# Performance work log

Hardware: AMD Instinct MI355X
Metric: run time of the kernel (lower is better)

The kernel has to match this reference:

```python
import jax, jax.numpy as jnp
import numpy as np

N_ATOM_FEATS = 64
N_RBF = 10
N_CONV = 3
N_HIDDEN = 64
N_NODES = 50000
N_EDGES = 800000
N_GRAPHS = 512


def setup_inputs() -> dict:
    key = jax.random.key(0)
    ks = jax.random.split(key, 32)
    d = {}
    d["x_ids"] = jax.random.randint(ks[0], (N_NODES,), 0, 95)
    d["edge_index"] = jax.random.randint(ks[1], (2, N_EDGES), 0, N_NODES)
    d["edge_attr"] = jax.random.uniform(ks[2], (N_EDGES,), jnp.float32) * 6.0  # distances in [0,6)
    d["batch"] = jnp.sort(jax.random.randint(ks[3], (N_NODES,), 0, N_GRAPHS))
    # parameters
    def lin(k, fan_in, shape):
        return jax.random.normal(k, shape, jnp.float32) / np.sqrt(fan_in)
    d["emb"] = jax.random.normal(ks[4], (95, N_ATOM_FEATS), jnp.float32)
    d["blk_W1"] = lin(ks[5], N_ATOM_FEATS, (N_CONV, N_ATOM_FEATS, N_ATOM_FEATS))
    d["blk_b1"] = jnp.zeros((N_CONV, N_ATOM_FEATS), jnp.float32)
    d["blk_We"] = lin(ks[6], N_RBF, (N_CONV, N_RBF, N_ATOM_FEATS))
    d["blk_be"] = jnp.zeros((N_CONV, N_ATOM_FEATS), jnp.float32)
    d["blk_W2"] = lin(ks[7], N_ATOM_FEATS, (N_CONV, N_ATOM_FEATS, N_ATOM_FEATS))
    d["blk_b2"] = jnp.zeros((N_CONV, N_ATOM_FEATS), jnp.float32)
    d["Ws"] = lin(ks[8], N_ATOM_FEATS, (N_ATOM_FEATS, 2 * N_HIDDEN))
    d["bs"] = jnp.zeros((2 * N_HIDDEN,), jnp.float32)
    d["Wbg1"] = lin(ks[9], 2 * N_HIDDEN, (2 * N_HIDDEN, N_HIDDEN))
    d["bbg1"] = jnp.zeros((N_HIDDEN,), jnp.float32)
    d["Wbg2"] = lin(ks[10], N_HIDDEN, (N_HIDDEN, 1))
    d["bbg2"] = jnp.zeros((1,), jnp.float32)
    d["Weh1"] = lin(ks[11], 2 * N_HIDDEN, (2 * N_HIDDEN, N_HIDDEN))
    d["beh1"] = jnp.zeros((N_HIDDEN,), jnp.float32)
    d["Weh2"] = lin(ks[12], N_HIDDEN, (N_HIDDEN, 1))
    d["beh2"] = jnp.zeros((1,), jnp.float32)
    return d


def reference(x_ids, edge_index, edge_attr, batch, emb,
              blk_W1, blk_b1, blk_We, blk_be, blk_W2, blk_b2,
              Ws, bs, Wbg1, bbg1, Wbg2, bbg2, Weh1, beh1, Weh2, beh2):
    src, dst = edge_index[0], edge_index[1]
    # embedding lookup [N, F]
    x = emb[x_ids]
    # Gaussian smearing RBF: [E, n_rbf]
    offset = jnp.linspace(0.0, 6.0, N_RBF).astype(edge_attr.dtype)
    coeff = -0.5 / (offset[1] - offset[0]) ** 2
    e = jnp.exp(coeff * (edge_attr[:, None] - offset) ** 2)
    # interaction blocks (SchNet-style CFConv with residual)
    for i in range(N_CONV):
        h = x @ blk_W1[i] + blk_b1[i]                     # [N, F]
        f = e @ blk_We[i] + blk_be[i]                     # [E, F] edge filters
        m = h[src] * f                                    # [E, F] messages
        agg = jax.ops.segment_sum(m, dst, num_segments=N_NODES)
        x = x + agg @ blk_W2[i] + blk_b2[i]
        x = jax.nn.softplus(x)
    # global mean pool over graphs
    sums = jax.ops.segment_sum(x, batch, num_segments=N_GRAPHS)
    cnts = jax.ops.segment_sum(jnp.ones((x.shape[0],), x.dtype), batch, num_segments=N_GRAPHS)
    c = sums / jnp.maximum(cnts, 1.0)[:, None]
    c = jax.nn.relu(c @ Ws + bs)                          # [G, 2H]
    out_bg = jax.nn.relu(c @ Wbg1 + bbg1) @ Wbg2 + bbg2   # [G, 1]
    out_eh = jax.nn.relu(c @ Weh1 + beh1) @ Weh2 + beh2   # [G, 1]
    return (out_bg, out_eh)
```

## Files before the change

kernel.cpp:

```cpp
#include <hip/hip_runtime.h>
#include <hip/hip_fp16.h>
#include <cstddef>


#define BSH 8

#define RBF_C0 1.0f
#define RBF_C1 0.60653065971f
#define RBF_C2 0.13533528324f
#define RBF_C3 0.011108996538f
#define RBF_C4 3.3546262790e-4f
#define RBF_C5 3.7266531720e-6f
#define RBF_C6 1.5229979745e-8f
#define RBF_C7 2.2897348457e-11f
#define RBF_C8 1.2664165549e-14f
#define RBF_C9 2.5767043600e-18f

__device__ __forceinline__ float softplusf(float v) {
    return fmaxf(v, 0.0f) + log1pf(__expf(-fabsf(v)));
}

__device__ __forceinline__ float row_gemv(const float4* __restrict__ xr,
                                          const float w[64], float bj) {
    float a0 = bj, a1 = 0.f, a2 = 0.f, a3 = 0.f;
#pragma unroll
    for (int q = 0; q < 4; ++q) {
        float4 v0 = xr[4 * q + 0], v1 = xr[4 * q + 1];
        float4 v2 = xr[4 * q + 2], v3 = xr[4 * q + 3];
        a0 = fmaf(v0.x, w[16 * q + 0], a0);  a0 = fmaf(v0.y, w[16 * q + 1], a0);
        a0 = fmaf(v0.z, w[16 * q + 2], a0);  a0 = fmaf(v0.w, w[16 * q + 3], a0);
        a1 = fmaf(v1.x, w[16 * q + 4], a1);  a1 = fmaf(v1.y, w[16 * q + 5], a1);
        a1 = fmaf(v1.z, w[16 * q + 6], a1);  a1 = fmaf(v1.w, w[16 * q + 7], a1);
        a2 = fmaf(v2.x, w[16 * q + 8], a2);  a2 = fmaf(v2.y, w[16 * q + 9], a2);
        a2 = fmaf(v2.z, w[16 * q + 10], a2); a2 = fmaf(v2.w, w[16 * q + 11], a2);
        a3 = fmaf(v3.x, w[16 * q + 12], a3); a3 = fmaf(v3.y, w[16 * q + 13], a3);
        a3 = fmaf(v3.z, w[16 * q + 14], a3); a3 = fmaf(v3.w, w[16 * q + 15], a3);
    }
    return (a0 + a1) + (a2 + a3);
}

__device__ __forceinline__ float filt_ab(const float wp[10], float bj, float A, float B) {
    float P = wp[9];
    P = fmaf(B, P, wp[8]); P = fmaf(B, P, wp[7]); P = fmaf(B, P, wp[6]);
    P = fmaf(B, P, wp[5]); P = fmaf(B, P, wp[4]); P = fmaf(B, P, wp[3]);
    P = fmaf(B, P, wp[2]); P = fmaf(B, P, wp[1]); P = fmaf(B, P, wp[0]);
    return fmaf(A, P, bj);
}

__global__ void k_pre(const int* __restrict__ dst, int* __restrict__ deg,
                      const int* __restrict__ batch, int* __restrict__ gstart,
                      const int* __restrict__ ids, const float* __restrict__ emb,
                      const float* __restrict__ W1, const float* __restrict__ b1,
                      float* __restrict__ x, __half* __restrict__ hA,
                      int n_edges, int n_nodes, int n_graphs) {
    int tid = blockIdx.x * blockDim.x + threadIdx.x;
    int nth = gridDim.x * blockDim.x;
    for (int e = tid; e < n_edges; e += nth) atomicAdd(&deg[dst[e]], 1);
    for (int n = tid; n < n_nodes; n += nth) {
        int b = batch[n];
        int prev = (n == 0) ? -1 : batch[n - 1];
        for (int g = prev + 1; g <= b; ++g) gstart[g] = n;
        if (n == n_nodes - 1)
            for (int g = b + 1; g <= n_graphs; ++g) gstart[g] = n_nodes;
    }
    int lane = threadIdx.x & 63;
    int gw = __builtin_amdgcn_readfirstlane(tid >> 6);
    int nw = nth >> 6;
    float w[64];
#pragma unroll
    for (int k = 0; k < 64; ++k) w[k] = W1[k * 64 + lane];
    float bj = b1[lane];
    for (int n = gw; n < n_nodes; n += nw) {
        int id = __builtin_amdgcn_readfirstlane(ids[n]);
        const float4* xr = (const float4*)(emb + id * 64);
        float v = row_gemv(xr, w, bj);
        x[n * 64 + lane] = emb[id * 64 + lane];
        hA[n * 64 + lane] = __float2half(v);
    }
}

__global__ void k_scana(const int* __restrict__ deg, int* __restrict__ off_,
                        int* __restrict__ bsum, int n) {
    __shared__ int s[256];
    int i = blockIdx.x * 256 + threadIdx.x;
    int v = (i < n) ? deg[i] : 0;
    s[threadIdx.x] = v;
    __syncthreads();
    for (int off = 1; off < 256; off <<= 1) {
        int t = (threadIdx.x >= off) ? s[threadIdx.x - off] : 0;
        __syncthreads();
        s[threadIdx.x] += t;
        __syncthreads();
    }
    if (i < n) off_[i + 1] = s[threadIdx.x];
    if (threadIdx.x == 255) bsum[blockIdx.x] = s[255];
}

__global__ void k_scanb(int* __restrict__ bsum, int nb) {
    __shared__ int s[256];
    int v = ((int)threadIdx.x < nb) ? bsum[threadIdx.x] : 0;
    s[threadIdx.x] = v;
    __syncthreads();
    for (int off = 1; off < 256; off <<= 1) {
        int t = (threadIdx.x >= off) ? s[threadIdx.x - off] : 0;
        __syncthreads();
        s[threadIdx.x] += t;
        __syncthreads();
    }
    if ((int)threadIdx.x < nb) bsum[threadIdx.x] = s[threadIdx.x] - v;
}

__global__ void k_scanc(const int* __restrict__ deg, const int* __restrict__ bsum,
                        int* __restrict__ off_, int* __restrict__ cursor,
                        int* __restrict__ bcursor, int n) {
    int i = blockIdx.x * blockDim.x + threadIdx.x;
    if (i < n) {
        int incl = off_[i + 1] + bsum[i >> 8];
        off_[i + 1] = incl;
        cursor[i] = incl - deg[i];
        if (((i + 1) & ((1 << BSH) - 1)) == 0)
            bcursor[(i + 1) >> BSH] = incl;
    }
    if (i == 0) { off_[0] = 0; bcursor[0] = 0; }
}

__global__ __launch_bounds__(256) void k_scat1(
        const int* __restrict__ src, const int* __restrict__ dst,
        const float* __restrict__ dist, int* __restrict__ bcursor,
        int4* __restrict__ tmp, int n_edges) {
    __shared__ int hist[256], sofs[256], hbase[256], lcur[256];
    __shared__ int4 buf[1024];
    const int t = threadIdx.x;
    const int base = blockIdx.x << 10;

    hist[t] = 0;
    __syncthreads();

    int bk[4]; int4 pl[4];
#pragma unroll
    for (int i = 0; i < 4; ++i) {
        int e = base + (i << 8) + t;
        if (e < n_edges) {
            int d_ = dst[e];
            float dd = dist[e];
            float A = __expf(-1.125f * dd * dd);
            float B = __expf(1.5f * dd);
            pl[i] = make_int4(src[e] << 6, __float_as_int(A), __float_as_int(B), d_);
            bk[i] = d_ >> BSH;
            atomicAdd(&hist[bk[i]], 1);
        } else bk[i] = -1;
    }
    __syncthreads();

    int mycnt = hist[t];
    for (int off = 1; off < 256; off <<= 1) {
        int v = (t >= off) ? hist[t - off] : 0;
        __syncthreads();
        hist[t] += v;
        __syncthreads();
    }
    sofs[t] = hist[t] - mycnt;
    lcur[t] = hist[t] - mycnt;
    if (mycnt > 0) hbase[t] = atomicAdd(&bcursor[t], mycnt);
    __syncthreads();

#pragma unroll
    for (int i = 0; i < 4; ++i) {
        if (bk[i] >= 0) {
            int ls = atomicAdd(&lcur[bk[i]], 1);
            buf[ls] = pl[i];
        }
    }
    __syncthreads();

    int tot = n_edges - base; if (tot > 1024) tot = 1024;
    for (int s = t; s < tot; s += 256) {
        int4 p = buf[s];
        int b = p.w >> BSH;
        tmp[hbase[b] + (s - sofs[b])] = p;
    }
}

__global__ __launch_bounds__(256) void k_scat2(
        const int4* __restrict__ tmp, const int* __restrict__ off_,
        int* __restrict__ cursor, int4* __restrict__ psort, int n_nodes) {
    int b = blockIdx.x;
    int s0 = off_[b << BSH];
    int hi = (b + 1) << BSH; if (hi > n_nodes) hi = n_nodes;
    int s1 = off_[hi];
    int s = s0 + threadIdx.x;
    for (; s + 768 < s1; s += 1024) {
        int4 p0 = tmp[s], p1 = tmp[s + 256], p2 = tmp[s + 512], p3 = tmp[s + 768];
        int q0 = atomicAdd(&cursor[p0.w], 1);
        int q1 = atomicAdd(&cursor[p1.w], 1);
        int q2 = atomicAdd(&cursor[p2.w], 1);
        int q3 = atomicAdd(&cursor[p3.w], 1);
        psort[q0] = p0; psort[q1] = p1; psort[q2] = p2; psort[q3] = p3;
    }
    for (; s < s1; s += 256) {
        int4 p = tmp[s];
        psort[atomicAdd(&cursor[p.w], 1)] = p;
    }
}

__global__ void k_scatter(const int* __restrict__ src, const int* __restrict__ dst,
                          const float* __restrict__ dist, int* __restrict__ cursor,
                          int4* __restrict__ psort, int n_edges) {
    int e = blockIdx.x * blockDim.x + threadIdx.x;
    if (e >= n_edges) return;
    int t = dst[e];
    int pos = atomicAdd(&cursor[t], 1);
    float d = dist[e];
    float A = __expf(-1.125f * d * d);
    float B = __expf(1.5f * d);
    psort[pos] = make_int4(src[e] << 6, __float_as_int(A), __float_as_int(B), 0);
}

__global__ __launch_bounds__(256, 8) void k_gather(
        const int4* __restrict__ ps, const int* __restrict__ off,
        const __half* __restrict__ h,
        const float* __restrict__ We, const float* __restrict__ be,
        float* __restrict__ agg, int n_nodes) {
    int lane = threadIdx.x & 63;
    int gw = __builtin_amdgcn_readfirstlane((blockIdx.x * blockDim.x + threadIdx.x) >> 6);
    int nw = (gridDim.x * blockDim.x) >> 6;

    const float C[10] = {RBF_C0, RBF_C1, RBF_C2, RBF_C3, RBF_C4,
                         RBF_C5, RBF_C6, RBF_C7, RBF_C8, RBF_C9};
    float wp[10];
#pragma unroll
    for (int r = 0; r < 10; ++r) wp[r] = We[r * 64 + lane] * C[r];
    float bj = be[lane];

    for (int n = gw; n < n_nodes; n += nw) {
        int k0 = off[n], k1 = off[n + 1];
        float acc = 0.0f;
        int k = k0;
        for (; k + 8 <= k1; k += 8) {
            int4 p0 = ps[k + 0], p1 = ps[k + 1], p2 = ps[k + 2], p3 = ps[k + 3];
            int4 p4 = ps[k + 4], p5 = ps[k + 5], p6 = ps[k + 6], p7 = ps[k + 7];
            float g0 = __half2float(h[p0.x + lane]);
            float g1 = __half2float(h[p1.x + lane]);
            float g2 = __half2float(h[p2.x + lane]);
            float g3 = __half2float(h[p3.x + lane]);
            float g4 = __half2float(h[p4.x + lane]);
            float g5 = __half2float(h[p5.x + lane]);
            float g6 = __half2float(h[p6.x + lane]);
            float g7 = __half2float(h[p7.x + lane]);
            acc = fmaf(g0, filt_ab(wp, bj, __int_as_float(p0.y), __int_as_float(p0.z)), acc);
            acc = fmaf(g1, filt_ab(wp, bj, __int_as_float(p1.y), __int_as_float(p1.z)), acc);
            acc = fmaf(g2, filt_ab(wp, bj, __int_as_float(p2.y), __int_as_float(p2.z)), acc);
            acc = fmaf(g3, filt_ab(wp, bj, __int_as_float(p3.y), __int_as_float(p3.z)), acc);
            acc = fmaf(g4, filt_ab(wp, bj, __int_as_float(p4.y), __int_as_float(p4.z)), acc);
            acc = fmaf(g5, filt_ab(wp, bj, __int_as_float(p5.y), __int_as_float(p5.z)), acc);
            acc = fmaf(g6, filt_ab(wp, bj, __int_as_float(p6.y), __int_as_float(p6.z)), acc);
            acc = fmaf(g7, filt_ab(wp, bj, __int_as_float(p7.y), __int_as_float(p7.z)), acc);
        }
        for (; k + 4 <= k1; k += 4) {
            int4 p0 = ps[k + 0], p1 = ps[k + 1], p2 = ps[k + 2], p3 = ps[k + 3];
            float g0 = __half2float(h[p0.x + lane]);
            float g1 = __half2float(h[p1.x + lane]);
            float g2 = __half2float(h[p2.x + lane]);
            float g3 = __half2float(h[p3.x + lane]);
            acc = fmaf(g0, filt_ab(wp, bj, __int_as_float(p0.y), __int_as_float(p0.z)), acc);
            acc = fmaf(g1, filt_ab(wp, bj, __int_as_float(p1.y), __int_as_float(p1.z)), acc);
            acc = fmaf(g2, filt_ab(wp, bj, __int_as_float(p2.y), __int_as_float(p2.z)), acc);
            acc = fmaf(g3, filt_ab(wp, bj, __int_as_float(p3.y), __int_as_float(p3.z)), acc);
        }
        for (; k < k1; ++k) {
            int4 p = ps[k];
            float g = __half2float(h[p.x + lane]);
            acc = fmaf(g, filt_ab(wp, bj, __int_as_float(p.y), __int_as_float(p.z)), acc);
        }
        agg[n * 64 + lane] = acc;
    }
}

__global__ __launch_bounds__(256) void k_epi(
        const float* __restrict__ agg, float* __restrict__ x,
        const float* __restrict__ W2, const float* __restrict__ b2,
        const float* __restrict__ W1n, const float* __restrict__ b1n,
        __half* __restrict__ hout, int n_nodes, int do_next) {
    __shared__ float B1[64 * 65];
    const int t = threadIdx.x;
    const int lane = t & 63;
    const int wid = __builtin_amdgcn_readfirstlane(t >> 6);
    const int base = blockIdx.x << 6;
    const int nv = min(64, n_nodes - base);

#pragma unroll
    for (int i = 0; i < 4; ++i) {
        int f = ((wid * 4 + i) << 8) + (lane << 2);
        int r = f >> 6, c = f & 63;
        int rs = min(r, nv - 1);
        const float4 v = *(const float4*)(agg + (((size_t)(base + rs)) << 6) + c);
        B1[r * 65 + c + 0] = v.x; B1[r * 65 + c + 1] = v.y;
        B1[r * 65 + c + 2] = v.z; B1[r * 65 + c + 3] = v.w;
    }
    __syncthreads();

    float o[16];
#pragma unroll
    for (int jj = 0; jj < 16; ++jj) o[jj] = 0.0f;
#pragma unroll 4
    for (int k = 0; k < 64; ++k) {
        float a = B1[lane * 65 + k];
        const float* w = W2 + (k << 6) + (wid << 4);
#pragma unroll
        for (int jj = 0; jj < 16; ++jj) o[jj] = fmaf(a, w[jj], o[jj]);
    }
    __syncthreads();

#pragma unroll
    for (int i = 0; i < 4; ++i) {
        int f = ((wid * 4 + i) << 8) + (lane << 2);
        int r = f >> 6, c = f & 63;
        int rs = min(r, nv - 1);
        const float4 v = *(const float4*)(x + (((size_t)(base + rs)) << 6) + c);
        B1[r * 65 + c + 0] = v.x; B1[r * 65 + c + 1] = v.y;
        B1[r * 65 + c + 2] = v.z; B1[r * 65 + c + 3] = v.w;
    }
    __syncthreads();

#pragma unroll
    for (int jj = 0; jj < 16; ++jj) {
        int j = (wid << 4) + jj;
        float xv = B1[lane * 65 + j];
        float xn = softplusf(xv + o[jj] + b2[j]);
        B1[lane * 65 + j] = xn;
    }
    __syncthreads();

#pragma unroll
    for (int rr = 0; rr < 16; ++rr) {
        int r = (wid << 4) + rr;
        if (r < nv) x[(((size_t)(base + r)) << 6) + lane] = B1[r * 65 + lane];
    }

    if (do_next) {
        float o2[16];
#pragma unroll
        for (int jj = 0; jj < 16; ++jj) o2[jj] = b1n[(wid << 4) + jj];
#pragma unroll 4
        for (int k = 0; k < 64; ++k) {
            float xk = B1[lane * 65 + k];
            const float* w = W1n + (k << 6) + (wid << 4);
#pragma unroll
            for (int jj = 0; jj < 16; ++jj) o2[jj] = fmaf(xk, w[jj], o2[jj]);
        }
        __syncthreads();
#pragma unroll
        for (int jj = 0; jj < 16; ++jj)
            B1[lane * 65 + (wid << 4) + jj] = o2[jj];
        __syncthreads();
#pragma unroll
        for (int rr = 0; rr < 16; ++rr) {
            int r = (wid << 4) + rr;
            if (r < nv)
                hout[(((size_t)(base + r)) << 6) + lane] = __float2half(B1[r * 65 + lane]);
        }
    }
}

__global__ __launch_bounds__(256, 6) void k_conv(
        const int4* __restrict__ ps, const int* __restrict__ off,
        const __half* __restrict__ h,
        const float* __restrict__ We, const float* __restrict__ be,
        const float* __restrict__ W2, const float* __restrict__ b2,
        const float* __restrict__ W1n, const float* __restrict__ b1n,
        float* __restrict__ x, __half* __restrict__ hout,
        int n_nodes, int do_next) {
    int lane = threadIdx.x & 63;
    int gw = __builtin_amdgcn_readfirstlane((blockIdx.x * blockDim.x + threadIdx.x) >> 6);
    int nw = (gridDim.x * blockDim.x) >> 6;

    const float C[10] = {RBF_C0, RBF_C1, RBF_C2, RBF_C3, RBF_C4,
                         RBF_C5, RBF_C6, RBF_C7, RBF_C8, RBF_C9};
    float wp[10];
#pragma unroll
    for (int r = 0; r < 10; ++r) wp[r] = We[r * 64 + lane] * C[r];
    float bj  = be[lane];
    float b2j = b2[lane];
    float b1j = do_next ? b1n[lane] : 0.0f;

    for (int n = gw; n < n_nodes; n += nw) {
        int k0 = off[n], k1 = off[n + 1];
        float acc = 0.0f;
        int k = k0;
        for (; k + 8 <= k1; k += 8) {
            int4 p0 = ps[k + 0], p1 = ps[k + 1], p2 = ps[k + 2], p3 = ps[k + 3];
            int4 p4 = ps[k + 4], p5 = ps[k + 5], p6 = ps[k + 6], p7 = ps[k + 7];
            float g0 = __half2float(h[p0.x + lane]);
            float g1 = __half2float(h[p1.x + lane]);
            float g2 = __half2float(h[p2.x + lane]);
            float g3 = __half2float(h[p3.x + lane]);
            float g4 = __half2float(h[p4.x + lane]);
            float g5 = __half2float(h[p5.x + lane]);
            float g6 = __half2float(h[p6.x + lane]);
            float g7 = __half2float(h[p7.x + lane]);
            acc = fmaf(g0, filt_ab(wp, bj, __int_as_float(p0.y), __int_as_float(p0.z)), acc);
            acc = fmaf(g1, filt_ab(wp, bj, __int_as_float(p1.y), __int_as_float(p1.z)), acc);
            acc = fmaf(g2, filt_ab(wp, bj, __int_as_float(p2.y), __int_as_float(p2.z)), acc);
            acc = fmaf(g3, filt_ab(wp, bj, __int_as_float(p3.y), __int_as_float(p3.z)), acc);
            acc = fmaf(g4, filt_ab(wp, bj, __int_as_float(p4.y), __int_as_float(p4.z)), acc);
            acc = fmaf(g5, filt_ab(wp, bj, __int_as_float(p5.y), __int_as_float(p5.z)), acc);
            acc = fmaf(g6, filt_ab(wp, bj, __int_as_float(p6.y), __int_as_float(p6.z)), acc);
            acc = fmaf(g7, filt_ab(wp, bj, __int_as_float(p7.y), __int_as_float(p7.z)), acc);
        }
        for (; k + 4 <= k1; k += 4) {
            int4 p0 = ps[k + 0], p1 = ps[k + 1], p2 = ps[k + 2], p3 = ps[k + 3];
            float g0 = __half2float(h[p0.x + lane]);
            float g1 = __half2float(h[p1.x + lane]);
            float g2 = __half2float(h[p2.x + lane]);
            float g3 = __half2float(h[p3.x + lane]);
            acc = fmaf(g0, filt_ab(wp, bj, __int_as_float(p0.y), __int_as_float(p0.z)), acc);
            acc = fmaf(g1, filt_ab(wp, bj, __int_as_float(p1.y), __int_as_float(p1.z)), acc);
            acc = fmaf(g2, filt_ab(wp, bj, __int_as_float(p2.y), __int_as_float(p2.z)), acc);
            acc = fmaf(g3, filt_ab(wp, bj, __int_as_float(p3.y), __int_as_float(p3.z)), acc);
        }
        for (; k < k1; ++k) {
            int4 p = ps[k];
            float g = __half2float(h[p.x + lane]);
            acc = fmaf(g, filt_ab(wp, bj, __int_as_float(p.y), __int_as_float(p.z)), acc);
        }
        float o0 = b2j + x[n * 64 + lane];
        float o1 = 0.f, o2 = 0.f, o3 = 0.f;
#pragma unroll 4
        for (int kk = 0; kk < 16; ++kk) {
            o0 = fmaf(__shfl(acc, kk),      W2[(kk)      * 64 + lane], o0);
            o1 = fmaf(__shfl(acc, kk + 16), W2[(kk + 16) * 64 + lane], o1);
            o2 = fmaf(__shfl(acc, kk + 32), W2[(kk + 32) * 64 + lane], o2);
            o3 = fmaf(__shfl(acc, kk + 48), W2[(kk + 48) * 64 + lane], o3);
        }
        float xn = softplusf((o0 + o1) + (o2 + o3));
        x[n * 64 + lane] = xn;
        if (do_next) {
            float q0 = b1j, q1 = 0.f, q2 = 0.f, q3 = 0.f;
#pragma unroll 4
            for (int kk = 0; kk < 16; ++kk) {
                q0 = fmaf(__shfl(xn, kk),      W1n[(kk)      * 64 + lane], q0);
                q1 = fmaf(__shfl(xn, kk + 16), W1n[(kk + 16) * 64 + lane], q1);
                q2 = fmaf(__shfl(xn, kk + 32), W1n[(kk + 32) * 64 + lane], q2);
                q3 = fmaf(__shfl(xn, kk + 48), W1n[(kk + 48) * 64 + lane], q3);
            }
            hout[n * 64 + lane] = __float2half((q0 + q1) + (q2 + q3));
        }
    }
}

__global__ void k_poolhead(const float* __restrict__ x, const int* __restrict__ gstart,
                           const float* __restrict__ Ws, const float* __restrict__ bs,
                           const float* __restrict__ Wbg1, const float* __restrict__ bbg1,
                           const float* __restrict__ Wbg2, const float* __restrict__ bbg2,
                           const float* __restrict__ Weh1, const float* __restrict__ beh1,
                           const float* __restrict__ Weh2, const float* __restrict__ beh2,
                           float* __restrict__ out, int n_graphs) {
    __shared__ float red[256];
    __shared__ float c[64];
    __shared__ float h1[128];
    int g = blockIdx.x;
    int t = threadIdx.x, j = t & 63, part = t >> 6;
    int s0 = gstart[g], s1 = gstart[g + 1];
    float acc = 0.0f;
    for (int n = s0 + part; n < s1; n += 4) acc += x[n * 64 + j];
    red[t] = acc;
    __syncthreads();
    if (part == 0)
        c[j] = (red[j] + red[64 + j] + red[128 + j] + red[192 + j]) /
               fmaxf((float)(s1 - s0), 1.0f);
    __syncthreads();
    if (t < 128) {
        float av = bs[t];
#pragma unroll 8
        for (int k = 0; k < 64; ++k) av = fmaf(c[k], Ws[k * 128 + t], av);
        h1[t] = fmaxf(av, 0.0f);
    }
    __syncthreads();
    if (t < 128) {
        const float* W1p = (t < 64) ? Wbg1 : Weh1;
        const float* b1p = (t < 64) ? bbg1 : beh1;
        const float* W2p = (t < 64) ? Wbg2 : Weh2;
        float b2v = (t < 64) ? bbg2[0] : beh2[0];
        int ln = t & 63;
        float a2 = b1p[ln];
#pragma unroll 8
        for (int k = 0; k < 128; ++k) a2 = fmaf(h1[k], W1p[k * 64 + ln], a2);
        a2 = fmaxf(a2, 0.0f);
        float pr = a2 * W2p[ln];
#pragma unroll
        for (int off = 32; off > 0; off >>= 1) pr += __shfl_down(pr, off);
        if (ln == 0) out[(t < 64 ? 0 : n_graphs) + g] = pr + b2v;
    }
}

extern "C" void kernel_launch(void* const* d_in, const int* in_sizes, int n_in,
                              void* d_out, int out_size, void* d_ws, size_t ws_size,
                              hipStream_t stream) {
    const int*   x_ids = (const int*)d_in[0];
    const int*   eidx  = (const int*)d_in[1];
    const float* eattr = (const float*)d_in[2];
    const int*   batch = (const int*)d_in[3];
    const float* emb   = (const float*)d_in[4];
    const float* W1    = (const float*)d_in[5];
    const float* b1    = (const float*)d_in[6];
    const float* We    = (const float*)d_in[7];
    const float* be    = (const float*)d_in[8];
    const float* W2    = (const float*)d_in[9];
    const float* b2    = (const float*)d_in[10];
    const float* Ws_   = (const float*)d_in[11];
    const float* bs_   = (const float*)d_in[12];
    const float* Wbg1  = (const float*)d_in[13];
    const float* bbg1  = (const float*)d_in[14];
    const float* Wbg2  = (const float*)d_in[15];
    const float* bbg2  = (const float*)d_in[16];
    const float* Weh1  = (const float*)d_in[17];
    const float* beh1  = (const float*)d_in[18];
    const float* Weh2  = (const float*)d_in[19];
    const float* beh2  = (const float*)d_in[20];

    int n_nodes  = in_sizes[0];
    int n_edges  = in_sizes[2];
    int n_graphs = out_size / 2;
    const int* src = eidx;
    const int* dst = eidx + n_edges;
    int nbuck = (n_nodes + (1 << BSH) - 1) >> BSH;
    int nbc = (nbuck < 256 ? 256 : nbuck) + 4;

    size_t base_bytes =
        (size_t)n_nodes * 64 * sizeof(float)
      + (size_t)n_nodes * 64 * sizeof(__half) * 2
      + (size_t)n_edges * sizeof(int4)
      + (size_t)n_nodes * sizeof(int) * 2
      + (size_t)(n_nodes + 1) * sizeof(int)
      + 256 * sizeof(int)
      + (size_t)(n_graphs + 1) * sizeof(int)
      + (size_t)nbc * sizeof(int);
    size_t agg_bytes = (size_t)n_nodes * 64 * sizeof(float);
    size_t tmp_bytes = (size_t)n_edges * sizeof(int4);
    size_t aggtmp_bytes = agg_bytes > tmp_bytes ? agg_bytes : tmp_bytes;
    int use_split = (ws_size >= base_bytes + aggtmp_bytes + 1024) ? 1 : 0;

    char* p = (char*)d_ws;
    float* x     = (float*)p;   p += (size_t)n_nodes * 64 * sizeof(float);
    __half* hA   = (__half*)p;  p += (size_t)n_nodes * 64 * sizeof(__half);
    __half* hB   = (__half*)p;  p += (size_t)n_nodes * 64 * sizeof(__half);
    int4* psort  = (int4*)p;    p += (size_t)n_edges * sizeof(int4);
    int* deg     = (int*)p;     p += (size_t)n_nodes * sizeof(int);
    int* off_    = (int*)p;     p += (size_t)(n_nodes + 1) * sizeof(int);
    int* cursor  = (int*)p;     p += (size_t)n_nodes * sizeof(int);
    int* bsum    = (int*)p;     p += 256 * sizeof(int);
    int* gstart  = (int*)p;     p += (size_t)(n_graphs + 1) * sizeof(int);
    int* bcursor = (int*)p;     p += (size_t)nbc * sizeof(int);
    float* agg   = (float*)p;
    int4* tmp    = (int4*)p;
    float* out   = (float*)d_out;

    int nchunks = (n_nodes + 255) / 256;
    int nbE = (n_edges + 255) / 256;
    int nbN = (n_nodes + 255) / 256;
    int ntile = (n_nodes + 63) / 64;
    int nbS1 = (n_edges + 1023) / 1024;

    hipMemsetAsync(deg, 0, (size_t)n_nodes * sizeof(int), stream);
    k_pre<<<nbE, 256, 0, stream>>>(dst, deg, batch, gstart, x_ids, emb, W1, b1,
                                   x, hA, n_edges, n_nodes, n_graphs);
    k_scana<<<nchunks, 256, 0, stream>>>(deg, off_, bsum, n_nodes);
    k_scanb<<<1, 256, 0, stream>>>(bsum, nchunks);
    k_scanc<<<nbN, 256, 0, stream>>>(deg, bsum, off_, cursor, bcursor, n_nodes);

    if (use_split) {
        k_scat1<<<nbS1, 256, 0, stream>>>(src, dst, eattr, bcursor, tmp, n_edges);
        k_scat2<<<nbuck, 256, 0, stream>>>(tmp, off_, cursor, psort, n_nodes);
        k_gather<<<4096, 256, 0, stream>>>(psort, off_, hA, We, be, agg, n_nodes);
        k_epi<<<ntile, 256, 0, stream>>>(agg, x, W2, b2,
                                         W1 + 4096, b1 + 64, hB, n_nodes, 1);
        k_gather<<<4096, 256, 0, stream>>>(psort, off_, hB, We + 640, be + 64, agg, n_nodes);
        k_epi<<<ntile, 256, 0, stream>>>(agg, x, W2 + 4096, b2 + 64,
                                         W1 + 8192, b1 + 128, hA, n_nodes, 1);
        k_gather<<<4096, 256, 0, stream>>>(psort, off_, hA, We + 1280, be + 128, agg, n_nodes);
        k_epi<<<ntile, 256, 0, stream>>>(agg, x, W2 + 8192, b2 + 128,
                                         nullptr, nullptr, nullptr, n_nodes, 0);
    } else {
        k_scatter<<<nbE, 256, 0, stream>>>(src, dst, eattr, cursor, psort, n_edges);
        k_conv<<<4096, 256, 0, stream>>>(psort, off_, hA, We, be, W2, b2,
                                         W1 + 4096, b1 + 64, x, hB, n_nodes, 1);
        k_conv<<<4096, 256, 0, stream>>>(psort, off_, hB, We + 640, be + 64,
                                         W2 + 4096, b2 + 64,
                                         W1 + 8192, b1 + 128, x, hA, n_nodes, 1);
        k_conv<<<4096, 256, 0, stream>>>(psort, off_, hA, We + 1280, be + 128,
                                         W2 + 8192, b2 + 128,
                                         nullptr, nullptr, x, nullptr, n_nodes, 0);
    }

    k_poolhead<<<n_graphs, 256, 0, stream>>>(x, gstart, Ws_, bs_, Wbg1, bbg1, Wbg2, bbg2,
                                             Weh1, beh1, Weh2, beh2, out, n_graphs);
}
```

Baseline: 384.6 us.

## Rewrite epilogue as wave-per-node GEMV with register-resident weights

The node epilogue kernel changes from a 64-node shared-memory tile, where W2 and W1 are streamed from global memory for every k, to a persistent grid-stride design. Each lane holds one output column of W2 and W1 in registers, and each wave processes one node row at a time using broadcast float4 loads of the agg row. It removes the shared-memory tile transposes and the block barriers. The cost is about 128 extra VGPRs per thread, which may cut occupancy, and each wave now handles one node at a time with redundant row loads across lanes.

```diff
diff --git a/kernel.cpp b/kernel.cpp
--- a/kernel.cpp
+++ b/kernel.cpp
@@ -27,6 +27,24 @@
     for (int q = 0; q < 4; ++q) {
         float4 v0 = xr[4 * q + 0], v1 = xr[4 * q + 1];
         float4 v2 = xr[4 * q + 2], v3 = xr[4 * q + 3];
+        a0 = fmaf(v0.x, w[16 * q + 0], a0);  a0 = fmaf(v0.y, w[16 * q + 1], a0);
+        a0 = fmaf(v0.z, w[16 * q + 2], a0);  a0 = fmaf(v0.w, w[16 * q + 3], a0);
+        a1 = fmaf(v1.x, w[16 * q + 4], a1);  a1 = fmaf(v1.y, w[16 * q + 5], a1);
+        a1 = fmaf(v1.z, w[16 * q + 6], a1);  a1 = fmaf(v1.w, w[16 * q + 7], a1);
+        a2 = fmaf(v2.x, w[16 * q + 8], a2);  a2 = fmaf(v2.y, w[16 * q + 9], a2);
+        a2 = fmaf(v2.z, w[16 * q + 10], a2); a2 = fmaf(v2.w, w[16 * q + 11], a2);
+        a3 = fmaf(v3.x, w[16 * q + 12], a3); a3 = fmaf(v3.y, w[16 * q + 13], a3);
+        a3 = fmaf(v3.z, w[16 * q + 14], a3); a3 = fmaf(v3.w, w[16 * q + 15], a3);
+    }
+    return (a0 + a1) + (a2 + a3);
+}
+
+__device__ __forceinline__ float row_gemv_l(const float* xr, const float w[64], float bj) {
+    float a0 = bj, a1 = 0.f, a2 = 0.f, a3 = 0.f;
+#pragma unroll
+    for (int q = 0; q < 4; ++q) {
+        float4 v0 = ((const float4*)xr)[4 * q + 0], v1 = ((const float4*)xr)[4 * q + 1];
+        float4 v2 = ((const float4*)xr)[4 * q + 2], v3 = ((const float4*)xr)[4 * q + 3];
         a0 = fmaf(v0.x, w[16 * q + 0], a0);  a0 = fmaf(v0.y, w[16 * q + 1], a0);
         a0 = fmaf(v0.z, w[16 * q + 2], a0);  a0 = fmaf(v0.w, w[16 * q + 3], a0);
         a1 = fmaf(v1.x, w[16 * q + 4], a1);  a1 = fmaf(v1.y, w[16 * q + 5], a1);
@@ -281,83 +299,34 @@
         const float* __restrict__ W2, const float* __restrict__ b2,
         const float* __restrict__ W1n, const float* __restrict__ b1n,
         __half* __restrict__ hout, int n_nodes, int do_next) {
-    __shared__ float B1[64 * 65];
-    const int t = threadIdx.x;
-    const int lane = t & 63;
-    const int wid = __builtin_amdgcn_readfirstlane(t >> 6);
-    const int base = blockIdx.x << 6;
-    const int nv = min(64, n_nodes - base);
-
-#pragma unroll
-    for (int i = 0; i < 4; ++i) {
-        int f = ((wid * 4 + i) << 8) + (lane << 2);
-        int r = f >> 6, c = f & 63;
-        int rs = min(r, nv - 1);
-        const float4 v = *(const float4*)(agg + (((size_t)(base + rs)) << 6) + c);
-        B1[r * 65 + c + 0] = v.x; B1[r * 65 + c + 1] = v.y;
-        B1[r * 65 + c + 2] = v.z; B1[r * 65 + c + 3] = v.w;
-    }
-    __syncthreads();
-
-    float o[16];
-#pragma unroll
-    for (int jj = 0; jj < 16; ++jj) o[jj] = 0.0f;
-#pragma unroll 4
-    for (int k = 0; k < 64; ++k) {
-        float a = B1[lane * 65 + k];
-        const float* w = W2 + (k << 6) + (wid << 4);
-#pragma unroll
-        for (int jj = 0; jj < 16; ++jj) o[jj] = fmaf(a, w[jj], o[jj]);
-    }
-    __syncthreads();
-
-#pragma unroll
-    for (int i = 0; i < 4; ++i) {
-        int f = ((wid * 4 + i) << 8) + (lane << 2);
-        int r = f >> 6, c = f & 63;
-        int rs = min(r, nv - 1);
-        const float4 v = *(const float4*)(x + (((size_t)(base + rs)) << 6) + c);
-        B1[r * 65 + c + 0] = v.x; B1[r * 65 + c + 1] = v.y;
-        B1[r * 65 + c + 2] = v.z; B1[r * 65 + c + 3] = v.w;
-    }
-    __syncthreads();
-
-#pragma unroll
-    for (int jj = 0; jj < 16; ++jj) {
-        int j = (wid << 4) + jj;
-        float xv = B1[lane * 65 + j];
-        float xn = softplusf(xv + o[jj] + b2[j]);
-        B1[lane * 65 + j] = xn;
-    }
-    __syncthreads();
-
-#pragma unroll
-    for (int rr = 0; rr < 16; ++rr) {
-        int r = (wid << 4) + rr;
-        if (r < nv) x[(((size_t)(base + r)) << 6) + lane] = B1[r * 65 + lane];
-    }
-
+    __shared__ float xrow[4][72];
+    const int lane = threadIdx.x & 63;
+    const int wid = threadIdx.x >> 6;
+    int gw = (blockIdx.x * blockDim.x + threadIdx.x) >> 6;
+    int nw = (gridDim.x * blockDim.x) >> 6;
+
+    float w2[64];
+#pragma unroll
+    for (int k = 0; k < 64; ++k) w2[k] = W2[k * 64 + lane];
+    float b2j = b2[lane];
+    float w1[64];
+    float b1j = 0.0f;
     if (do_next) {
-        float o2[16];
-#pragma unroll
-        for (int jj = 0; jj < 16; ++jj) o2[jj] = b1n[(wid << 4) + jj];
-#pragma unroll 4
-        for (int k = 0; k < 64; ++k) {
-            float xk = B1[lane * 65 + k];
-            const float* w = W1n + (k << 6) + (wid << 4);
-#pragma unroll
-            for (int jj = 0; jj < 16; ++jj) o2[jj] = fmaf(xk, w[jj], o2[jj]);
-        }
-        __syncthreads();
-#pragma unroll
-        for (int jj = 0; jj < 16; ++jj)
-            B1[lane * 65 + (wid << 4) + jj] = o2[jj];
-        __syncthreads();
-#pragma unroll
-        for (int rr = 0; rr < 16; ++rr) {
-            int r = (wid << 4) + rr;
-            if (r < nv)
-                hout[(((size_t)(base + r)) << 6) + lane] = __float2half(B1[r * 65 + lane]);
+#pragma unroll
+        for (int k = 0; k < 64; ++k) w1[k] = W1n[k * 64 + lane];
+        b1j = b1n[lane];
+    }
+    float* myrow = xrow[wid];
+
+    for (int n = gw; n < n_nodes; n += nw) {
+        const float4* ar = (const float4*)(agg + ((size_t)n << 6));
+        float o = row_gemv(ar, w2, b2j) + x[((size_t)n << 6) + lane];
+        float xn = softplusf(o);
+        x[((size_t)n << 6) + lane] = xn;
+        if (do_next) {
+            myrow[lane] = xn;
+            float hv = row_gemv_l(myrow, w1, b1j);
+            hout[((size_t)n << 6) + lane] = __float2half(hv);
         }
     }
 }
@@ -558,7 +527,6 @@
     int nchunks = (n_nodes + 255) / 256;
     int nbE = (n_edges + 255) / 256;
     int nbN = (n_nodes + 255) / 256;
-    int ntile = (n_nodes + 63) / 64;
     int nbS1 = (n_edges + 1023) / 1024;
 
     hipMemsetAsync(deg, 0, (size_t)n_nodes * sizeof(int), stream);
@@ -572,14 +540,14 @@
         k_scat1<<<nbS1, 256, 0, stream>>>(src, dst, eattr, bcursor, tmp, n_edges);
         k_scat2<<<nbuck, 256, 0, stream>>>(tmp, off_, cursor, psort, n_nodes);
         k_gather<<<4096, 256, 0, stream>>>(psort, off_, hA, We, be, agg, n_nodes);
-        k_epi<<<ntile, 256, 0, stream>>>(agg, x, W2, b2,
-                                         W1 + 4096, b1 + 64, hB, n_nodes, 1);
+        k_epi<<<1024, 256, 0, stream>>>(agg, x, W2, b2,
+                                        W1 + 4096, b1 + 64, hB, n_nodes, 1);
         k_gather<<<4096, 256, 0, stream>>>(psort, off_, hB, We + 640, be + 64, agg, n_nodes);
-        k_epi<<<ntile, 256, 0, stream>>>(agg, x, W2 + 4096, b2 + 64,
-                                         W1 + 8192, b1 + 128, hA, n_nodes, 1);
+        k_epi<<<1024, 256, 0, stream>>>(agg, x, W2 + 4096, b2 + 64,
+                                        W1 + 8192, b1 + 128, hA, n_nodes, 1);
         k_gather<<<4096, 256, 0, stream>>>(psort, off_, hA, We + 1280, be + 128, agg, n_nodes);
-        k_epi<<<ntile, 256, 0, stream>>>(agg, x, W2 + 8192, b2 + 128,
-                                         nullptr, nullptr, nullptr, n_nodes, 0);
+        k_epi<<<1024, 256, 0, stream>>>(agg, x, W2 + 8192, b2 + 128,
+                                        nullptr, nullptr, nullptr, n_nodes, 0);
     } else {
         k_scatter<<<nbE, 256, 0, stream>>>(src, dst, eattr, cursor, psort, n_edges);
         k_conv<<<4096, 256, 0, stream>>>(psort, off_, hA, We, be, W2, b2,
```

Result: slower. 432.6 us (+12.5%).

## Fuse edge gather into node epilogue kernel, drop agg buffer round-trip

Applied to the files above, without the earlier changes.

Merges the per-node edge gather and the dense epilogue into one kernel. Each 64-node tile first computes its aggregated messages straight into shared memory, then applies W2, softplus and the next layer's W1. This removes the fp32 agg array write and read and one launch per conv layer. In exchange the gather phase runs with one block per tile instead of a 4096-block grid-stride loop with higher occupancy bounds, so latency hiding and load balance may suffer. Weight loads in the small GEMMs are also vectorized to float4.

```diff
diff --git a/kernel.cpp b/kernel.cpp
--- a/kernel.cpp
+++ b/kernel.cpp
@@ -216,71 +216,14 @@
     psort[pos] = make_int4(src[e] << 6, __float_as_int(A), __float_as_int(B), 0);
 }
 
-__global__ __launch_bounds__(256, 8) void k_gather(
+__global__ __launch_bounds__(256) void k_convf(
         const int4* __restrict__ ps, const int* __restrict__ off,
         const __half* __restrict__ h,
         const float* __restrict__ We, const float* __restrict__ be,
-        float* __restrict__ agg, int n_nodes) {
-    int lane = threadIdx.x & 63;
-    int gw = __builtin_amdgcn_readfirstlane((blockIdx.x * blockDim.x + threadIdx.x) >> 6);
-    int nw = (gridDim.x * blockDim.x) >> 6;
-
-    const float C[10] = {RBF_C0, RBF_C1, RBF_C2, RBF_C3, RBF_C4,
-                         RBF_C5, RBF_C6, RBF_C7, RBF_C8, RBF_C9};
-    float wp[10];
-#pragma unroll
-    for (int r = 0; r < 10; ++r) wp[r] = We[r * 64 + lane] * C[r];
-    float bj = be[lane];
-
-    for (int n = gw; n < n_nodes; n += nw) {
-        int k0 = off[n], k1 = off[n + 1];
-        float acc = 0.0f;
-        int k = k0;
-        for (; k + 8 <= k1; k += 8) {
-            int4 p0 = ps[k + 0], p1 = ps[k + 1], p2 = ps[k + 2], p3 = ps[k + 3];
-            int4 p4 = ps[k + 4], p5 = ps[k + 5], p6 = ps[k + 6], p7 = ps[k + 7];
-            float g0 = __half2float(h[p0.x + lane]);
-            float g1 = __half2float(h[p1.x + lane]);
-            float g2 = __half2float(h[p2.x + lane]);
-            float g3 = __half2float(h[p3.x + lane]);
-            float g4 = __half2float(h[p4.x + lane]);
-            float g5 = __half2float(h[p5.x + lane]);
-            float g6 = __half2float(h[p6.x + lane]);
-            float g7 = __half2float(h[p7.x + lane]);
-            acc = fmaf(g0, filt_ab(wp, bj, __int_as_float(p0.y), __int_as_float(p0.z)), acc);
-            acc = fmaf(g1, filt_ab(wp, bj, __int_as_float(p1.y), __int_as_float(p1.z)), acc);
-            acc = fmaf(g2, filt_ab(wp, bj, __int_as_float(p2.y), __int_as_float(p2.z)), acc);
-            acc = fmaf(g3, filt_ab(wp, bj, __int_as_float(p3.y), __int_as_float(p3.z)), acc);
-            acc = fmaf(g4, filt_ab(wp, bj, __int_as_float(p4.y), __int_as_float(p4.z)), acc);
-            acc = fmaf(g5, filt_ab(wp, bj, __int_as_float(p5.y), __int_as_float(p5.z)), acc);
-            acc = fmaf(g6, filt_ab(wp, bj, __int_as_float(p6.y), __int_as_float(p6.z)), acc);
-            acc = fmaf(g7, filt_ab(wp, bj, __int_as_float(p7.y), __int_as_float(p7.z)), acc);
-        }
-        for (; k + 4 <= k1; k += 4) {
-            int4 p0 = ps[k + 0], p1 = ps[k + 1], p2 = ps[k + 2], p3 = ps[k + 3];
-            float g0 = __half2float(h[p0.x + lane]);
-            float g1 = __half2float(h[p1.x + lane]);
-            float g2 = __half2float(h[p2.x + lane]);
-            float g3 = __half2float(h[p3.x + lane]);
-            acc = fmaf(g0, filt_ab(wp, bj, __int_as_float(p0.y), __int_as_float(p0.z)), acc);
-            acc = fmaf(g1, filt_ab(wp, bj, __int_as_float(p1.y), __int_as_float(p1.z)), acc);
-            acc = fmaf(g2, filt_ab(wp, bj, __int_as_float(p2.y), __int_as_float(p2.z)), acc);
-            acc = fmaf(g3, filt_ab(wp, bj, __int_as_float(p3.y), __int_as_float(p3.z)), acc);
-        }
-        for (; k < k1; ++k) {
-            int4 p = ps[k];
-            float g = __half2float(h[p.x + lane]);
-            acc = fmaf(g, filt_ab(wp, bj, __int_as_float(p.y), __int_as_float(p.z)), acc);
-        }
-        agg[n * 64 + lane] = acc;
-    }
-}
-
-__global__ __launch_bounds__(256) void k_epi(
-        const float* __restrict__ agg, float* __restrict__ x,
         const float* __restrict__ W2, const float* __restrict__ b2,
         const float* __restrict__ W1n, const float* __restrict__ b1n,
-        __half* __restrict__ hout, int n_nodes, int do_next) {
+        float* __restrict__ x, __half* __restrict__ hout,
+        int n_nodes, int do_next) {
     __shared__ float B1[64 * 65];
     const int t = threadIdx.x;
     const int lane = t & 63;
@@ -288,14 +231,58 @@
     const int base = blockIdx.x << 6;
     const int nv = min(64, n_nodes - base);
 
-#pragma unroll
-    for (int i = 0; i < 4; ++i) {
-        int f = ((wid * 4 + i) << 8) + (lane << 2);
-        int r = f >> 6, c = f & 63;
-        int rs = min(r, nv - 1);
-        const float4 v = *(const float4*)(agg + (((size_t)(base + rs)) << 6) + c);
-        B1[r * 65 + c + 0] = v.x; B1[r * 65 + c + 1] = v.y;
-        B1[r * 65 + c + 2] = v.z; B1[r * 65 + c + 3] = v.w;
+    const float C[10] = {RBF_C0, RBF_C1, RBF_C2, RBF_C3, RBF_C4,
+                         RBF_C5, RBF_C6, RBF_C7, RBF_C8, RBF_C9};
+    float wp[10];
+#pragma unroll
+    for (int r = 0; r < 10; ++r) wp[r] = We[r * 64 + lane] * C[r];
+    float bj = be[lane];
+
+    for (int i = 0; i < 16; ++i) {
+        int rloc = (wid << 4) + i;
+        int n = base + rloc;
+        float acc = 0.0f;
+        if (n < n_nodes) {
+            int k0 = off[n], k1 = off[n + 1];
+            int k = k0;
+            for (; k + 8 <= k1; k += 8) {
+                int4 p0 = ps[k + 0], p1 = ps[k + 1], p2 = ps[k + 2], p3 = ps[k + 3];
+                int4 p4 = ps[k + 4], p5 = ps[k + 5], p6 = ps[k + 6], p7 = ps[k + 7];
+                float g0 = __half2float(h[p0.x + lane]);
+                float g1 = __half2float(h[p1.x + lane]);
+                float g2 = __half2float(h[p2.x + lane]);
+                float g3 = __half2float(h[p3.x + lane]);
+                float g4 = __half2float(h[p4.x + lane]);
+                float g5 = __half2float(h[p5.x + lane]);
+                float g6 = __half2float(h[p6.x + lane]);
+                float g7 = __half2float(h[p7.x + lane]);
+                acc = fmaf(g0, filt_ab(wp, bj, __int_as_float(p0.y), __int_as_float(p0.z)), acc);
+                acc = fmaf(g1, filt_ab(wp, bj, __int_as_float(p1.y), __int_as_float(p1.z)), acc);
+                acc = fmaf(g2, filt_ab(wp, bj, __int_as_float(p2.y), __int_as_float(p2.z)), acc);
+                acc = fmaf(g3, filt_ab(wp, bj, __int_as_float(p3.y), __int_as_float(p3.z)), acc);
+                acc = fmaf(g4, filt_ab(wp, bj, __int_as_float(p4.y), __int_as_float(p4.z)), acc);
+                acc = fmaf(g5, filt_ab(wp, bj, __int_as_float(p5.y), __int_as_float(p5.z)), acc);
+                acc = fmaf(g6, filt_ab(wp, bj, __int_as_float(p6.y), __int_as_float(p6.z)), acc);
+                acc = fmaf(g7, filt_ab(wp, bj, __int_as_float(p7.y), __int_as_float(p7.z)), acc);
+            }
+            for (; k + 4 <= k1; k += 4) {
+                int4 p0 = ps[k + 0], p1 = ps[k + 1], p2 = ps[k + 2], p3 = ps[k + 3];
+                float g0 = __half2float(h[p0.x + lane]);
+                float g1 = __half2float(h[p1.x + lane]);
+                float g2 = __half2float(h[p2.x + lane]);
+                float g3 = __half2float(h[p3.x + lane]);
+                acc = fmaf(g0, filt_ab(wp, bj, __int_as_float(p0.y), __int_as_float(p0.z)), acc);
+                acc = fmaf(g1, filt_ab(wp, bj, __int_as_float(p1.y), __int_as_float(p1.z)), acc);
+                acc = fmaf(g2, filt_ab(wp, bj, __int_as_float(p2.y), __int_as_float(p2.z)), acc);
+                acc = fmaf(g3, filt_ab(wp, bj, __int_as_float(p3.y), __int_as_float(p3.z)), acc);
+            }
+            for (; k < k1; ++k) {
+                int4 p = ps[k];
+                float g = __half2float(h[p.x + lane]);
+                acc = fmaf(g, filt_ab(wp, bj, __int_as_float(p.y), __int_as_float(p.z)), acc);
+            }
+        }
+        B1[rloc * 65 + lane] = acc;
     }
     __syncthreads();
 
@@ -305,9 +292,16 @@
 #pragma unroll 4
     for (int k = 0; k < 64; ++k) {
         float a = B1[lane * 65 + k];
-        const float* w = W2 + (k << 6) + (wid << 4);
-#pragma unroll
-        for (int jj = 0; jj < 16; ++jj) o[jj] = fmaf(a, w[jj], o[jj]);
+        const float4* w4 = (const float4*)(W2 + (k << 6) + (wid << 4));
+        float4 wa = w4[0], wb = w4[1], wc = w4[2], wd = w4[3];
+        o[0]  = fmaf(a, wa.x, o[0]);  o[1]  = fmaf(a, wa.y, o[1]);
+        o[2]  = fmaf(a, wa.z, o[2]);  o[3]  = fmaf(a, wa.w, o[3]);
+        o[4]  = fmaf(a, wb.x, o[4]);  o[5]  = fmaf(a, wb.y, o[5]);
+        o[6]  = fmaf(a, wb.z, o[6]);  o[7]  = fmaf(a, wb.w, o[7]);
+        o[8]  = fmaf(a, wc.x, o[8]);  o[9]  = fmaf(a, wc.y, o[9]);
+        o[10] = fmaf(a, wc.z, o[10]); o[11] = fmaf(a, wc.w, o[11]);
+        o[12] = fmaf(a, wd.x, o[12]); o[13] = fmaf(a, wd.y, o[13]);
+        o[14] = fmaf(a, wd.z, o[14]); o[15] = fmaf(a, wd.w, o[15]);
     }
     __syncthreads();
 
@@ -344,9 +338,16 @@
 #pragma unroll 4
         for (int k = 0; k < 64; ++k) {
             float xk = B1[lane * 65 + k];
-            const float* w = W1n + (k << 6) + (wid << 4);
-#pragma unroll
-            for (int jj = 0; jj < 16; ++jj) o2[jj] = fmaf(xk, w[jj], o2[jj]);
+            const float4* w4 = (const float4*)(W1n + (k << 6) + (wid << 4));
+            float4 wa = w4[0], wb = w4[1], wc = w4[2], wd = w4[3];
+            o2[0]  = fmaf(xk, wa.x, o2[0]);  o2[1]  = fmaf(xk, wa.y, o2[1]);
+            o2[2]  = fmaf(xk, wa.z, o2[2]);  o2[3]  = fmaf(xk, wa.w, o2[3]);
+            o2[4]  = fmaf(xk, wb.x, o2[4]);  o2[5]  = fmaf(xk, wb.y, o2[5]);
+            o2[6]  = fmaf(xk, wb.z, o2[6]);  o2[7]  = fmaf(xk, wb.w, o2[7]);
+            o2[8]  = fmaf(xk, wc.x, o2[8]);  o2[9]  = fmaf(xk, wc.y, o2[9]);
+            o2[10] = fmaf(xk, wc.z, o2[10]); o2[11] = fmaf(xk, wc.w, o2[11]);
+            o2[12] = fmaf(xk, wd.x, o2[12]); o2[13] = fmaf(xk, wd.y, o2[13]);
+            o2[14] = fmaf(xk, wd.z, o2[14]); o2[15] = fmaf(xk, wd.w, o2[15]);
         }
         __syncthreads();
 #pragma unroll
@@ -535,10 +536,8 @@
       + 256 * sizeof(int)
       + (size_t)(n_graphs + 1) * sizeof(int)
       + (size_t)nbc * sizeof(int);
-    size_t agg_bytes = (size_t)n_nodes * 64 * sizeof(float);
     size_t tmp_bytes = (size_t)n_edges * sizeof(int4);
-    size_t aggtmp_bytes = agg_bytes > tmp_bytes ? agg_bytes : tmp_bytes;
-    int use_split = (ws_size >= base_bytes + aggtmp_bytes + 1024) ? 1 : 0;
+    int use_split = (ws_size >= base_bytes + tmp_bytes + 1024) ? 1 : 0;
 
     char* p = (char*)d_ws;
     float* x     = (float*)p;   p += (size_t)n_nodes * 64 * sizeof(float);
@@ -551,7 +550,6 @@
     int* bsum    = (int*)p;     p += 256 * sizeof(int);
     int* gstart  = (int*)p;     p += (size_t)(n_graphs + 1) * sizeof(int);
     int* bcursor = (int*)p;     p += (size_t)nbc * sizeof(int);
-    float* agg   = (float*)p;
     int4* tmp    = (int4*)p;
     float* out   = (float*)d_out;
 
@@ -571,15 +569,14 @@
     if (use_split) {
         k_scat1<<<nbS1, 256, 0, stream>>>(src, dst, eattr, bcursor, tmp, n_edges);
         k_scat2<<<nbuck, 256, 0, stream>>>(tmp, off_, cursor, psort, n_nodes);
-        k_gather<<<4096, 256, 0, stream>>>(psort, off_, hA, We, be, agg, n_nodes);
-        k_epi<<<ntile, 256, 0, stream>>>(agg, x, W2, b2,
-                                         W1 + 4096, b1 + 64, hB, n_nodes, 1);
-        k_gather<<<4096, 256, 0, stream>>>(psort, off_, hB, We + 640, be + 64, agg, n_nodes);
-        k_epi<<<ntile, 256, 0, stream>>>(agg, x, W2 + 4096, b2 + 64,
-                                         W1 + 8192, b1 + 128, hA, n_nodes, 1);
-        k_gather<<<4096, 256, 0, stream>>>(psort, off_, hA, We + 1280, be + 128, agg, n_nodes);
-        k_epi<<<ntile, 256, 0, stream>>>(agg, x, W2 + 8192, b2 + 128,
-                                         nullptr, nullptr, nullptr, n_nodes, 0);
+        k_convf<<<ntile, 256, 0, stream>>>(psort, off_, hA, We, be, W2, b2,
+                                           W1 + 4096, b1 + 64, x, hB, n_nodes, 1);
+        k_convf<<<ntile, 256, 0, stream>>>(psort, off_, hB, We + 640, be + 64,
+                                           W2 + 4096, b2 + 64,
+                                           W1 + 8192, b1 + 128, x, hA, n_nodes, 1);
+        k_convf<<<ntile, 256, 0, stream>>>(psort, off_, hA, We + 1280, be + 128,
+                                           W2 + 8192, b2 + 128,
+                                           nullptr, nullptr, x, nullptr, n_nodes, 0);
     } else {
         k_scatter<<<nbE, 256, 0, stream>>>(src, dst, eattr, cursor, psort, n_edges);
         k_conv<<<4096, 256, 0, stream>>>(psort, off_, hA, We, be, W2, b2,
```

Result: slower. 418.6 us (+8.8%).
